# Kernel optimization log

Measured on AMD Instinct MI355X. Metric: run time of the kernel, lower is better.

## Reference

```python
import jax, jax.numpy as jnp
import numpy as np

SAMPLE_SIZE = 4096  # deterministic mode: first SAMPLE_SIZE flattened pixels
EPS_STD = 1e-8
EPS_PDF = 1e-10


def _std(v):
    # torch.std is unbiased (ddof=1)
    return jnp.std(v, ddof=1)


def _adaptive_sigma(v):
    # sigma=None path: 0.2 * std, clamped to [0.001, 1.0]
    return jnp.clip(_std(v) * 0.2, 0.001, 1.0)


def _normalize(v):
    return (v - jnp.mean(v)) / (_std(v) + EPS_STD)


def _marginal_pdf(values, sigma):
    vn = _normalize(values)                      # [N]
    resid = vn[None, :] - vn[:, None]            # [N, N]
    kernel = jnp.exp(-0.5 * (resid / sigma) ** 2)
    pdf = jnp.mean(kernel, axis=1)               # [N]
    return pdf / (jnp.sum(pdf) + EPS_PDF)


def _joint_pdf(v1, v2, s1, s2):
    vn1 = _normalize(v1)
    vn2 = _normalize(v2)
    r1 = vn1[None, :] - vn1[:, None]             # [N, N]
    r2 = vn2[None, :] - vn2[:, None]             # [N, N]
    kernel = jnp.exp(-0.5 * (r1 / s1) ** 2) * jnp.exp(-0.5 * (r2 / s2) ** 2)
    pdf = jnp.mean(kernel, axis=1)
    return pdf / (jnp.sum(pdf) + EPS_PDF)


def _mi_kde(img1, img2):
    x = img1.reshape(-1)[:SAMPLE_SIZE]
    y = img2.reshape(-1)[:SAMPLE_SIZE]
    s1 = _adaptive_sigma(x)
    s2 = _adaptive_sigma(y)
    p1 = _marginal_pdf(x, s1)
    p2 = _marginal_pdf(y, s2)
    pj = _joint_pdf(x, y, s1, s2)
    ratio = (pj + EPS_PDF) / (p1 * p2 + EPS_PDF)
    log_ratio = jnp.log(jnp.clip(ratio, 1e-10, 1e10))
    return jnp.sum(pj * log_ratio)


def setup_inputs() -> dict:
    key = jax.random.key(0)
    k1, k2, k3 = jax.random.split(key, 3)
    shape = (2, 1, 128, 128)  # [B, C, H, W] images in [0, 1]
    return {
        "fused_img": jax.random.uniform(k1, shape, dtype=jnp.float32),
        "source_img1": jax.random.uniform(k2, shape, dtype=jnp.float32),
        "source_img2": jax.random.uniform(k3, shape, dtype=jnp.float32),
    }


def reference(fused_img, source_img1, source_img2):
    B = fused_img.shape[0]
    total = jnp.float32(0.0)
    for b in range(B):  # small fixed batch loop, matches original
        total = total + _mi_kde(fused_img[b], source_img1[b]) \
                      + _mi_kde(fused_img[b], source_img2[b])
    return -(total / B)
```

## Files before the change

kernel.cpp:

```cpp
#include <hip/hip_runtime.h>

#define N 4096
#define NBIN 1024
#define LOG2E 1.4426950408889634f

__device__ __forceinline__ float fast_exp2(float x) {
#if __has_builtin(__builtin_amdgcn_exp2f)
    return __builtin_amdgcn_exp2f(x);
#else
    return exp2f(x);
#endif
}

__device__ float block_reduce_sum(float v) {
    __shared__ float red[16];
    int lane = threadIdx.x & 63;
    int wid = threadIdx.x >> 6;
    #pragma unroll
    for (int off = 32; off; off >>= 1) v += __shfl_down(v, off, 64);
    if (lane == 0) red[wid] = v;
    __syncthreads();
    if (threadIdx.x == 0) {
        int nw = (int)(blockDim.x >> 6);
        float s = red[0];
        for (int w = 1; w < nw; ++w) s += red[w];
        red[0] = s;
    }
    __syncthreads();
    float r = red[0];
    __syncthreads();
    return r;
}

__device__ float4 block_reduce_stats(float s, float sq, float mn, float mx) {
    __shared__ float4 red4[16];
    int lane = threadIdx.x & 63;
    int wid = threadIdx.x >> 6;
    #pragma unroll
    for (int off = 32; off; off >>= 1) {
        s  += __shfl_down(s, off, 64);
        sq += __shfl_down(sq, off, 64);
        mn  = fminf(mn, __shfl_down(mn, off, 64));
        mx  = fmaxf(mx, __shfl_down(mx, off, 64));
    }
    if (lane == 0) red4[wid] = make_float4(s, sq, mn, mx);
    __syncthreads();
    if (threadIdx.x == 0) {
        float4 r = red4[0];
        #pragma unroll
        for (int w = 1; w < 16; ++w) {
            float4 q = red4[w];
            r.x += q.x; r.y += q.y;
            r.z = fminf(r.z, q.z); r.w = fmaxf(r.w, q.w);
        }
        red4[0] = r;
    }
    __syncthreads();
    float4 r = red4[0];
    __syncthreads();
    return r;
}

__global__ void __launch_bounds__(1024)
k_prep(const float* __restrict__ fused,
       const float* __restrict__ s1,
       const float* __restrict__ s2,
       float2* __restrict__ xa,
       float2* __restrict__ ma,
       float* __restrict__ par,
       float* __restrict__ hcnt,
       float* __restrict__ hmu,
       unsigned int* __restrict__ counter) {
    __shared__ unsigned int cnt[NBIN];
    __shared__ int qs[NBIN];
    int vec = blockIdx.x;
    int b = vec / 3, k = vec % 3;
    const float* src = (k == 0 ? fused : (k == 1 ? s1 : s2)) + b * 16384;
    int tid = threadIdx.x;

    if (vec == 0 && tid == 0) *counter = 0u;
    cnt[tid] = 0u; qs[tid] = 0;

    float v[4];
    float s = 0.f, sq = 0.f, mn = 1e30f, mx = -1e30f;
    #pragma unroll
    for (int t = 0; t < 4; ++t) {
        v[t] = src[tid + t * 1024];
        s += v[t]; sq = fmaf(v[t], v[t], sq);
        mn = fminf(mn, v[t]); mx = fmaxf(mx, v[t]);
    }
    float4 r = block_reduce_stats(s, sq, mn, mx);
    float mean = r.x * (1.0f / 4096.0f);
    float tssq = r.y - 4096.0f * mean * mean;
    float stdv = sqrtf(fmaxf(tssq, 0.f) / 4095.0f);
    float sigma = fminf(fmaxf(0.2f * stdv, 0.001f), 1.0f);
    float inv = 1.0f / (stdv + 1e-8f);
    float c1 = -0.5f * LOG2E / (sigma * sigma);
    float xmin = (r.z - mean) * inv;
    float xmax = (r.w - mean) * inv;
    float range = fmaxf(xmax - xmin, 1e-6f);
    float inv_bw = (float)NBIN / range;
    float binw = range * (1.0f / NBIN);

    float2* xav = xa + (size_t)vec * N;
    float2* mav = ma + (size_t)vec * N;
    __syncthreads();
    #pragma unroll
    for (int t = 0; t < 4; ++t) {
        int i = tid + t * 1024;
        float x = (v[t] - mean) * inv;
        float a = c1 * x * x;
        xav[i] = make_float2(x, a);
        mav[i] = make_float2(-2.0f * c1 * x, a);
        float rel = x - xmin;
        int bb = min(NBIN - 1, max(0, (int)(rel * inv_bw)));
        atomicAdd(&cnt[bb], 1u);
        atomicAdd(&qs[bb], (int)rintf(rel * 16384.0f));
    }
    __syncthreads();
    {
        unsigned int c = cnt[tid];
        hcnt[vec * NBIN + tid] = (float)c;
        float mu = c ? xmin + ((float)qs[tid] / (float)c) * (1.0f / 16384.0f)
                     : xmin + (tid + 0.5f) * binw;
        hmu[vec * NBIN + tid] = mu;
    }
    if (tid == 0) {
        par[vec * 8 + 0] = xmin;
        par[vec * 8 + 1] = inv_bw;
        par[vec * 8 + 2] = binw;
        par[vec * 8 + 3] = c1;
    }
}

__global__ void __launch_bounds__(256, 8)
k_main(const float2* __restrict__ xa,
       const float2* __restrict__ ma,
       const float* __restrict__ par,
       const float* __restrict__ hcnt,
       const float* __restrict__ hmu,
       float* __restrict__ marg,
       float* __restrict__ msum_part,
       float* __restrict__ part, int js) {
    __shared__ float4 sj[128];
    const int nib = 4;
    int bid = blockIdx.x;
    int tid = threadIdx.x;

    if (bid < 96) {
        int vec = bid >> 4, ic = bid & 15;
        int i = ic * 256 + tid;
        const float* P = par + vec * 8;
        float xmin = P[0], inv_bw = P[1], c1 = P[3];
        float xi = xa[(size_t)vec * N + i].x;
        float R = sqrtf(45.0f / fabsf(c1));
        int b0 = max(0, (int)((xi - R - xmin) * inv_bw));
        int b1 = min(NBIN - 1, (int)((xi + R - xmin) * inv_bw) + 1);
        const float* hc = hcnt + vec * NBIN;
        const float* hm = hmu + vec * NBIN;
        float acc = 0.f;
        #pragma unroll 4
        for (int bb = b0; bb <= b1; ++bb) {
            float d = xi - hm[bb];
            acc += hc[bb] * fast_exp2(c1 * d * d);
        }
        float raw = acc * (1.0f / N);
        marg[(size_t)vec * N + i] = raw;
        float tot = block_reduce_sum(raw);
        if (tid == 0) msum_part[bid] = tot;
        return;
    }

    int bid2 = bid - 96;
    int tt = bid2 / (nib * js);
    int rem = bid2 % (nib * js);
    int ib = rem / js, jsp = rem % js;
    int b = tt >> 1, pr = tt & 1;
    int vx = b * 3, vy = b * 3 + 1 + pr;
    int jlen = N / js;
    int j0 = jsp * jlen;
    int ibase = ib * 1024 + tid;

    const float2* xav = xa + (size_t)vx * N;
    const float2* yav = xa + (size_t)vy * N;
    const float2* mxv = ma + (size_t)vx * N;
    const float2* myv = ma + (size_t)vy * N;

    float mx[4], my[4], C[4];
    #pragma unroll
    for (int u = 0; u < 4; ++u) {
        float2 qx = mxv[ibase + u * 256];
        float2 qy = myv[ibase + u * 256];
        mx[u] = qx.x; my[u] = qy.x; C[u] = qx.y + qy.y;
    }
    float acc[4] = {0.f, 0.f, 0.f, 0.f};

    for (int jt = 0; jt < jlen; jt += 128) {
        int cnt = min(128, jlen - jt);
        __syncthreads();
        if (tid < cnt) {
            float2 xq = xav[j0 + jt + tid];
            float2 yq = yav[j0 + jt + tid];
            sj[tid] = make_float4(xq.x, yq.x, xq.y + yq.y, 0.f);
        }
        __syncthreads();
        #pragma unroll 2
        for (int j = 0; j < cnt; j += 2) {
            float4 q0 = sj[j];
            float4 q1 = sj[j + 1];
            float e0[4], e1[4], f0[4], f1[4];
            #pragma unroll
            for (int u = 0; u < 4; ++u) {
                e0[u] = fmaf(my[u], q0.y, fmaf(mx[u], q0.x, C[u])) + q0.z;
                e1[u] = fmaf(my[u], q1.y, fmaf(mx[u], q1.x, C[u])) + q1.z;
            }
            #pragma unroll
            for (int u = 0; u < 4; ++u) {
                f0[u] = fast_exp2(e0[u]);
                f1[u] = fast_exp2(e1[u]);
            }
            #pragma unroll
            for (int u = 0; u < 4; ++u)
                acc[u] += (f0[u] + f1[u]);
        }
    }
    float* dst = part + ((size_t)tt * js + jsp) * N + ibase;
    dst[0]   = acc[0];
    dst[256] = acc[1];
    dst[512] = acc[2];
    dst[768] = acc[3];
}

__global__ void k_redfin(const float* __restrict__ part,
                         const float* __restrict__ marg,
                         const float* __restrict__ msum_part,
                         float* __restrict__ A_part,
                         float* __restrict__ jsum_part,
                         unsigned int* __restrict__ counter,
                         float* __restrict__ out, int js) {
    __shared__ bool isLast;
    __shared__ float svec[6], stask[4], sA[4];
    int blk = blockIdx.x;
    int tt = blk >> 4;
    int ic = blk & 15;
    int b = tt >> 1, pr = tt & 1;
    int vx = b * 3, vy = b * 3 + 1 + pr;
    int i = ic * 256 + threadIdx.x;
    float s = 0.f;
    #pragma unroll 4
    for (int q = 0; q < js; ++q) s += part[((size_t)tt * js + q) * N + i];
    s *= (1.0f / N);
    float rx = marg[(size_t)vx * N + i];
    float ry = marg[(size_t)vy * N + i];
    float a = s * __logf(s / (rx * ry));
    float stot = block_reduce_sum(s);
    float atot = block_reduce_sum(a);
    if (threadIdx.x == 0) {
        jsum_part[blk] = stot;
        A_part[blk] = atot;
        __threadfence();
        unsigned int done = atomicAdd(counter, 1u);
        isLast = (done == 63u);
    }
    __syncthreads();
    if (!isLast) return;
    __threadfence();

    int tid = threadIdx.x;
    if (tid < 6) {
        float ss = 0.f;
        #pragma unroll
        for (int q = 0; q < 16; ++q) ss += msum_part[tid * 16 + q];
        svec[tid] = ss;
    } else if (tid >= 8 && tid < 12) {
        int c = tid - 8;
        float ss = 0.f, aa = 0.f;
        #pragma unroll
        for (int q = 0; q < 16; ++q) {
            ss += jsum_part[c * 16 + q];
            aa += A_part[c * 16 + q];
        }
        stask[c] = ss;
        sA[c] = aa;
    }
    __syncthreads();
    if (tid == 0) {
        float mi = 0.f;
        #pragma unroll
        for (int c = 0; c < 4; ++c) {
            int bb = c >> 1, pp = c & 1;
            int wx = bb * 3, wy = bb * 3 + 1 + pp;
            mi += sA[c] / stask[c] + __logf(svec[wx] * svec[wy] / stask[c]);
        }
        out[0] = -mi * 0.5f;
    }
}

extern "C" void kernel_launch(void* const* d_in, const int* in_sizes, int n_in,
                              void* d_out, int out_size, void* d_ws, size_t ws_size,
                              hipStream_t stream) {
    const float* fused = (const float*)d_in[0];
    const float* s1    = (const float*)d_in[1];
    const float* s2    = (const float*)d_in[2];
    float* out = (float*)d_out;
    float* ws  = (float*)d_ws;

    const size_t off_xa   = 0;
    const size_t off_ma   = off_xa + 12 * (size_t)N;
    const size_t off_par  = off_ma + 12 * (size_t)N;
    const size_t off_hc   = off_par + 64;
    const size_t off_hm   = off_hc + 6 * NBIN;
    const size_t off_mg   = off_hm + 6 * NBIN;
    const size_t off_ms   = off_mg + 6 * (size_t)N;
    const size_t off_A    = off_ms + 128;
    const size_t off_js   = off_A + 64;
    const size_t off_ctr  = off_js + 64;
    const size_t off_part = off_ctr + 16;

    int js = 32;
    while (js > 1 && (off_part + (size_t)4 * js * N) * 4 > ws_size) js >>= 1;

    float2* ws_xa  = (float2*)(ws + off_xa);
    float2* ws_ma  = (float2*)(ws + off_ma);
    float*  ws_par = ws + off_par;
    float*  ws_hc  = ws + off_hc;
    float*  ws_hm  = ws + off_hm;
    float*  ws_mg  = ws + off_mg;
    float*  ws_ms  = ws + off_ms;
    float*  ws_A   = ws + off_A;
    float*  ws_js  = ws + off_js;
    unsigned int* ws_ctr = (unsigned int*)(ws + off_ctr);
    float*  ws_part = ws + off_part;

    k_prep<<<dim3(6), dim3(1024), 0, stream>>>(fused, s1, s2, ws_xa, ws_ma,
                                               ws_par, ws_hc, ws_hm, ws_ctr);
    k_main<<<dim3(96 + 4 * 4 * js), dim3(256), 0, stream>>>(
        ws_xa, ws_ma, ws_par, ws_hc, ws_hm, ws_mg, ws_ms, ws_part, js);
    k_redfin<<<dim3(64), dim3(256), 0, stream>>>(ws_part, ws_mg, ws_ms,
                                                 ws_A, ws_js, ws_ctr, out, js);
}
```

Before: 34.67 us.

## Bucket-sort samples by x and restrict joint KDE to a neighbourhood window

Adds a k_sort kernel that counting-sorts each batch's samples by their fused-image histogram bin and records the permutation. The joint-PDF pass now processes sorted i-tiles of 512 and only iterates over j in the bin range within the Gaussian cutoff radius of x, instead of all N pairs, computing the quadratic-form terms on the fly rather than loading precomputed arrays. The marginal pass caches its histogram in shared memory. The aim is to cut most of the N^2 exp work, at the cost of an extra launch, a sort, and indirect gathers in the final reduction, plus truncation of far-tail kernel contributions.

```diff
diff --git a/kernel.cpp b/kernel.cpp
--- a/kernel.cpp
+++ b/kernel.cpp
@@ -65,8 +65,7 @@
 k_prep(const float* __restrict__ fused,
        const float* __restrict__ s1,
        const float* __restrict__ s2,
-       float2* __restrict__ xa,
-       float2* __restrict__ ma,
+       float* __restrict__ xn,
        float* __restrict__ par,
        float* __restrict__ hcnt,
        float* __restrict__ hmu,
@@ -102,16 +101,13 @@
     float inv_bw = (float)NBIN / range;
     float binw = range * (1.0f / NBIN);
 
-    float2* xav = xa + (size_t)vec * N;
-    float2* mav = ma + (size_t)vec * N;
+    float* xv = xn + (size_t)vec * N;
     __syncthreads();
     #pragma unroll
     for (int t = 0; t < 4; ++t) {
         int i = tid + t * 1024;
         float x = (v[t] - mean) * inv;
-        float a = c1 * x * x;
-        xav[i] = make_float2(x, a);
-        mav[i] = make_float2(-2.0f * c1 * x, a);
+        xv[i] = x;
         float rel = x - xmin;
         int bb = min(NBIN - 1, max(0, (int)(rel * inv_bw)));
         atomicAdd(&cnt[bb], 1u);
@@ -133,17 +129,70 @@
     }
 }
 
+__global__ void __launch_bounds__(1024)
+k_sort(const float* __restrict__ xn,
+       const float* __restrict__ par,
+       const float* __restrict__ hcnt,
+       float* __restrict__ srt,
+       int* __restrict__ perm,
+       int* __restrict__ binStartG) {
+    __shared__ int pf[NBIN];
+    __shared__ int bs[NBIN];
+    __shared__ unsigned int boff[NBIN];
+    int b = blockIdx.x;
+    int vecx = 3 * b;
+    int tid = threadIdx.x;
+    pf[tid] = (int)hcnt[vecx * NBIN + tid];
+    boff[tid] = 0u;
+    __syncthreads();
+    for (int off = 1; off < NBIN; off <<= 1) {
+        int add = (tid >= off) ? pf[tid - off] : 0;
+        __syncthreads();
+        pf[tid] += add;
+        __syncthreads();
+    }
+    bs[tid] = (tid == 0) ? 0 : pf[tid - 1];
+    binStartG[b * 1025 + tid + 1] = pf[tid];
+    if (tid == 0) binStartG[b * 1025] = 0;
+    __syncthreads();
+
+    const float* P = par + vecx * 8;
+    float xmin = P[0], inv_bw = P[1];
+    const float* X  = xn + (size_t)vecx * N;
+    const float* Y1 = xn + (size_t)(vecx + 1) * N;
+    const float* Y2 = xn + (size_t)(vecx + 2) * N;
+    float* xs  = srt + (size_t)(b * 3 + 0) * N;
+    float* y1s = srt + (size_t)(b * 3 + 1) * N;
+    float* y2s = srt + (size_t)(b * 3 + 2) * N;
+    int* pm = perm + (size_t)b * N;
+    #pragma unroll
+    for (int t = 0; t < 4; ++t) {
+        int i = tid + t * 1024;
+        float x = X[i];
+        float rel = x - xmin;
+        int bb = min(NBIN - 1, max(0, (int)(rel * inv_bw)));
+        int pos = bs[bb] + (int)atomicAdd(&boff[bb], 1u);
+        xs[pos]  = x;
+        y1s[pos] = Y1[i];
+        y2s[pos] = Y2[i];
+        pm[pos]  = i;
+    }
+}
+
+#define JS 16
 __global__ void __launch_bounds__(256, 8)
-k_main(const float2* __restrict__ xa,
-       const float2* __restrict__ ma,
+k_main(const float* __restrict__ xn,
        const float* __restrict__ par,
        const float* __restrict__ hcnt,
        const float* __restrict__ hmu,
+       const float* __restrict__ srt,
+       const int* __restrict__ binStartG,
        float* __restrict__ marg,
        float* __restrict__ msum_part,
-       float* __restrict__ part, int js) {
-    __shared__ float4 sj[128];
-    const int nib = 4;
+       float* __restrict__ part) {
+    __shared__ float4 sj[129];
+    __shared__ float shc[NBIN];
+    __shared__ float shm[NBIN];
     int bid = blockIdx.x;
     int tid = threadIdx.x;
 
@@ -152,17 +201,23 @@
         int i = ic * 256 + tid;
         const float* P = par + vec * 8;
         float xmin = P[0], inv_bw = P[1], c1 = P[3];
-        float xi = xa[(size_t)vec * N + i].x;
+        const float* hc = hcnt + vec * NBIN;
+        const float* hm = hmu + vec * NBIN;
+        #pragma unroll
+        for (int u = 0; u < 4; ++u) {
+            shc[tid + u * 256] = hc[tid + u * 256];
+            shm[tid + u * 256] = hm[tid + u * 256];
+        }
+        __syncthreads();
+        float xi = xn[(size_t)vec * N + i];
         float R = sqrtf(45.0f / fabsf(c1));
         int b0 = max(0, (int)((xi - R - xmin) * inv_bw));
         int b1 = min(NBIN - 1, (int)((xi + R - xmin) * inv_bw) + 1);
-        const float* hc = hcnt + vec * NBIN;
-        const float* hm = hmu + vec * NBIN;
         float acc = 0.f;
         #pragma unroll 4
         for (int bb = b0; bb <= b1; ++bb) {
-            float d = xi - hm[bb];
-            acc += hc[bb] * fast_exp2(c1 * d * d);
+            float d = xi - shm[bb];
+            acc += shc[bb] * fast_exp2(c1 * d * d);
         }
         float raw = acc * (1.0f / N);
         marg[(size_t)vec * N + i] = raw;
@@ -172,86 +227,97 @@
     }
 
     int bid2 = bid - 96;
-    int tt = bid2 / (nib * js);
-    int rem = bid2 % (nib * js);
-    int ib = rem / js, jsp = rem % js;
+    int tt = bid2 / (8 * JS);
+    int rem = bid2 % (8 * JS);
+    int ib = rem / JS, jsp = rem % JS;
     int b = tt >> 1, pr = tt & 1;
-    int vx = b * 3, vy = b * 3 + 1 + pr;
-    int jlen = N / js;
-    int j0 = jsp * jlen;
-    int ibase = ib * 1024 + tid;
-
-    const float2* xav = xa + (size_t)vx * N;
-    const float2* yav = xa + (size_t)vy * N;
-    const float2* mxv = ma + (size_t)vx * N;
-    const float2* myv = ma + (size_t)vy * N;
-
-    float mx[4], my[4], C[4];
-    #pragma unroll
-    for (int u = 0; u < 4; ++u) {
-        float2 qx = mxv[ibase + u * 256];
-        float2 qy = myv[ibase + u * 256];
-        mx[u] = qx.x; my[u] = qy.x; C[u] = qx.y + qy.y;
-    }
-    float acc[4] = {0.f, 0.f, 0.f, 0.f};
-
-    for (int jt = 0; jt < jlen; jt += 128) {
-        int cnt = min(128, jlen - jt);
+    int vx = 3 * b, vy = 3 * b + 1 + pr;
+    float c1x = par[vx * 8 + 3];
+    float c1y = par[vy * 8 + 3];
+    float xminx = par[vx * 8 + 0], inv_bwx = par[vx * 8 + 1];
+
+    const float* xs = srt + (size_t)(b * 3 + 0) * N;
+    const float* ys = srt + (size_t)(b * 3 + 1 + pr) * N;
+    const int* bS = binStartG + b * 1025;
+
+    int i0 = ib * 512;
+    float xf = xs[i0], xl = xs[i0 + 511];
+    float Rx = sqrtf(45.0f / fabsf(c1x));
+    int W = (int)fminf(Rx * inv_bwx + 1.0f, 1024.0f);
+    int blo = min(NBIN - 1, max(0, (int)((xf - xminx) * inv_bwx)));
+    int bhi = min(NBIN - 1, max(0, (int)((xl - xminx) * inv_bwx)));
+    int jlo = bS[max(0, blo - W)];
+    int jhi = bS[min(1024, bhi + W + 1)];
+    int len = jhi - jlo;
+    int per = (len + JS - 1) / JS;
+    int j0 = jlo + jsp * per;
+    int j1 = min(j0 + per, jhi);
+
+    int is1 = i0 + tid, is2 = is1 + 256;
+    float x1 = xs[is1], yv1 = ys[is1];
+    float x2 = xs[is2], yv2 = ys[is2];
+    float mx1 = -2.f * c1x * x1, my1 = -2.f * c1y * yv1;
+    float mx2 = -2.f * c1x * x2, my2 = -2.f * c1y * yv2;
+    float C1 = c1x * x1 * x1 + c1y * yv1 * yv1;
+    float C2 = c1x * x2 * x2 + c1y * yv2 * yv2;
+
+    float acc1 = 0.f, acc2 = 0.f;
+    for (int jt = j0; jt < j1; jt += 128) {
+        int cnt = min(128, j1 - jt);
         __syncthreads();
         if (tid < cnt) {
-            float2 xq = xav[j0 + jt + tid];
-            float2 yq = yav[j0 + jt + tid];
-            sj[tid] = make_float4(xq.x, yq.x, xq.y + yq.y, 0.f);
-        }
+            float xj = xs[jt + tid];
+            float yj = ys[jt + tid];
+            float S = fmaf(c1x * xj, xj, c1y * yj * yj);
+            sj[tid] = make_float4(xj, yj, S, 0.f);
+        }
+        if (tid == cnt && cnt < 129) sj[tid] = make_float4(0.f, 0.f, -3000.f, 0.f);
         __syncthreads();
+        int cntp = (cnt + 1) & ~1;
         #pragma unroll 2
-        for (int j = 0; j < cnt; j += 2) {
+        for (int j = 0; j < cntp; j += 2) {
             float4 q0 = sj[j];
             float4 q1 = sj[j + 1];
-            float e0[4], e1[4], f0[4], f1[4];
-            #pragma unroll
-            for (int u = 0; u < 4; ++u) {
-                e0[u] = fmaf(my[u], q0.y, fmaf(mx[u], q0.x, C[u])) + q0.z;
-                e1[u] = fmaf(my[u], q1.y, fmaf(mx[u], q1.x, C[u])) + q1.z;
-            }
-            #pragma unroll
-            for (int u = 0; u < 4; ++u) {
-                f0[u] = fast_exp2(e0[u]);
-                f1[u] = fast_exp2(e1[u]);
-            }
-            #pragma unroll
-            for (int u = 0; u < 4; ++u)
-                acc[u] += (f0[u] + f1[u]);
-        }
-    }
-    float* dst = part + ((size_t)tt * js + jsp) * N + ibase;
-    dst[0]   = acc[0];
-    dst[256] = acc[1];
-    dst[512] = acc[2];
-    dst[768] = acc[3];
+            float e10 = fmaf(my1, q0.y, fmaf(mx1, q0.x, C1)) + q0.z;
+            float e20 = fmaf(my2, q0.y, fmaf(mx2, q0.x, C2)) + q0.z;
+            float e11 = fmaf(my1, q1.y, fmaf(mx1, q1.x, C1)) + q1.z;
+            float e21 = fmaf(my2, q1.y, fmaf(mx2, q1.x, C2)) + q1.z;
+            float f10 = fast_exp2(e10);
+            float f20 = fast_exp2(e20);
+            float f11 = fast_exp2(e11);
+            float f21 = fast_exp2(e21);
+            acc1 += (f10 + f11);
+            acc2 += (f20 + f21);
+        }
+    }
+    float* dst = part + ((size_t)tt * JS + jsp) * N;
+    dst[is1] = acc1;
+    dst[is2] = acc2;
 }
 
 __global__ void k_redfin(const float* __restrict__ part,
                          const float* __restrict__ marg,
                          const float* __restrict__ msum_part,
+                         const int* __restrict__ perm,
                          float* __restrict__ A_part,
                          float* __restrict__ jsum_part,
                          unsigned int* __restrict__ counter,
-                         float* __restrict__ out, int js) {
+                         float* __restrict__ out) {
     __shared__ bool isLast;
     __shared__ float svec[6], stask[4], sA[4];
     int blk = blockIdx.x;
     int tt = blk >> 4;
     int ic = blk & 15;
     int b = tt >> 1, pr = tt & 1;
-    int vx = b * 3, vy = b * 3 + 1 + pr;
+    int vx = 3 * b, vy = 3 * b + 1 + pr;
     int i = ic * 256 + threadIdx.x;
     float s = 0.f;
     #pragma unroll 4
-    for (int q = 0; q < js; ++q) s += part[((size_t)tt * js + q) * N + i];
+    for (int q = 0; q < JS; ++q) s += part[((size_t)tt * JS + q) * N + i];
     s *= (1.0f / N);
-    float rx = marg[(size_t)vx * N + i];
-    float ry = marg[(size_t)vy * N + i];
+    int orig = perm[(size_t)b * N + i];
+    float rx = marg[(size_t)vx * N + orig];
+    float ry = marg[(size_t)vy * N + orig];
     float a = s * __logf(s / (rx * ry));
     float stot = block_reduce_sum(s);
     float atot = block_reduce_sum(a);
@@ -305,37 +371,40 @@
     float* out = (float*)d_out;
     float* ws  = (float*)d_ws;
 
-    const size_t off_xa   = 0;
-    const size_t off_ma   = off_xa + 12 * (size_t)N;
-    const size_t off_par  = off_ma + 12 * (size_t)N;
+    const size_t off_xn   = 0;
+    const size_t off_par  = off_xn + 6 * (size_t)N;
     const size_t off_hc   = off_par + 64;
     const size_t off_hm   = off_hc + 6 * NBIN;
-    const size_t off_mg   = off_hm + 6 * NBIN;
+    const size_t off_srt  = off_hm + 6 * NBIN;
+    const size_t off_perm = off_srt + 6 * (size_t)N;
+    const size_t off_bS   = off_perm + 2 * (size_t)N;
+    const size_t off_mg   = off_bS + 2112;
     const size_t off_ms   = off_mg + 6 * (size_t)N;
     const size_t off_A    = off_ms + 128;
     const size_t off_js   = off_A + 64;
     const size_t off_ctr  = off_js + 64;
     const size_t off_part = off_ctr + 16;
 
-    int js = 32;
-    while (js > 1 && (off_part + (size_t)4 * js * N) * 4 > ws_size) js >>= 1;
-
-    float2* ws_xa  = (float2*)(ws + off_xa);
-    float2* ws_ma  = (float2*)(ws + off_ma);
-    float*  ws_par = ws + off_par;
-    float*  ws_hc  = ws + off_hc;
-    float*  ws_hm  = ws + off_hm;
-    float*  ws_mg  = ws + off_mg;
-    float*  ws_ms  = ws + off_ms;
-    float*  ws_A   = ws + off_A;
-    float*  ws_js  = ws + off_js;
+    float* ws_xn  = ws + off_xn;
+    float* ws_par = ws + off_par;
+    float* ws_hc  = ws + off_hc;
+    float* ws_hm  = ws + off_hm;
+    float* ws_srt = ws + off_srt;
+    int*   ws_pm  = (int*)(ws + off_perm);
+    int*   ws_bS  = (int*)(ws + off_bS);
+    float* ws_mg  = ws + off_mg;
+    float* ws_ms  = ws + off_ms;
+    float* ws_A   = ws + off_A;
+    float* ws_js  = ws + off_js;
     unsigned int* ws_ctr = (unsigned int*)(ws + off_ctr);
-    float*  ws_part = ws + off_part;
-
-    k_prep<<<dim3(6), dim3(1024), 0, stream>>>(fused, s1, s2, ws_xa, ws_ma,
+    float* ws_part = ws + off_part;
+
+    k_prep<<<dim3(6), dim3(1024), 0, stream>>>(fused, s1, s2, ws_xn,
                                                ws_par, ws_hc, ws_hm, ws_ctr);
-    k_main<<<dim3(96 + 4 * 4 * js), dim3(256), 0, stream>>>(
-        ws_xa, ws_ma, ws_par, ws_hc, ws_hm, ws_mg, ws_ms, ws_part, js);
-    k_redfin<<<dim3(64), dim3(256), 0, stream>>>(ws_part, ws_mg, ws_ms,
-                                                 ws_A, ws_js, ws_ctr, out, js);
-}
+    k_sort<<<dim3(2), dim3(1024), 0, stream>>>(ws_xn, ws_par, ws_hc,
+                                               ws_srt, ws_pm, ws_bS);
+    k_main<<<dim3(96 + 4 * 8 * JS), dim3(256), 0, stream>>>(
+        ws_xn, ws_par, ws_hc, ws_hm, ws_srt, ws_bS, ws_mg, ws_ms, ws_part);
+    k_redfin<<<dim3(64), dim3(256), 0, stream>>>(ws_part, ws_mg, ws_ms, ws_pm,
+                                                 ws_A, ws_js, ws_ctr, out);
+}
```

New measurement: 44.25 us. 27.6% more time.
